# Performance work log

Measured on AMD Instinct MI355X. Metric: run time of the kernel, lower is better.

Reference implementation:

```python
import jax, jax.numpy as jnp
import numpy as np

N = 50000
E = 1600000
IN_CH = 64


def _sage_conv(x, edge_index, W_l, b_l, W_r):
    # PyG SAGEConv with mean aggregation:
    #   out = lin_l(mean_{j in N(i)} x_j) + lin_r(x_i)
    src, dst = edge_index[0], edge_index[1]
    n = x.shape[0]
    msg_sum = jax.ops.segment_sum(x[src], dst, num_segments=n)          # [N, d_in]
    cnt = jax.ops.segment_sum(jnp.ones((src.shape[0],), x.dtype), dst,
                              num_segments=n)                            # [N]
    agg = msg_sum / jnp.maximum(cnt, 1.0)[:, None]                       # mean, 0 if no nbrs
    return agg @ W_l.T + b_l + x @ W_r.T


def setup_inputs() -> dict:
    key = jax.random.key(0)
    ks = jax.random.split(key, 9)
    x = jax.random.normal(ks[0], (N, IN_CH), dtype=jnp.float32)
    edge_index = jax.random.randint(ks[1], (2, E), 0, N, dtype=jnp.int64)
    s = 1.0 / np.sqrt(IN_CH)
    W1_l = jax.random.uniform(ks[2], (64, IN_CH), jnp.float32, -s, s)
    b1_l = jnp.zeros((64,), jnp.float32)
    W1_r = jax.random.uniform(ks[3], (64, IN_CH), jnp.float32, -s, s)
    s2 = 1.0 / np.sqrt(64)
    W2_l = jax.random.uniform(ks[4], (32, 64), jnp.float32, -s2, s2)
    b2_l = jnp.zeros((32,), jnp.float32)
    W2_r = jax.random.uniform(ks[5], (32, 64), jnp.float32, -s2, s2)
    s3 = 1.0 / np.sqrt(32)
    W_lin = jax.random.uniform(ks[6], (1, 32), jnp.float32, -s3, s3)
    b_lin = jax.random.uniform(ks[7], (1,), jnp.float32, -s3, s3)
    return {"x": x, "edge_index": edge_index,
            "W1_l": W1_l, "b1_l": b1_l, "W1_r": W1_r,
            "W2_l": W2_l, "b2_l": b2_l, "W2_r": W2_r,
            "W_lin": W_lin, "b_lin": b_lin}


def reference(x, edge_index, W1_l, b1_l, W1_r, W2_l, b2_l, W2_r, W_lin, b_lin):
    h = jax.nn.relu(_sage_conv(x, edge_index, W1_l, b1_l, W1_r))   # [N, 64]
    h = jax.nn.relu(_sage_conv(h, edge_index, W2_l, b2_l, W2_r))   # [N, 32]
    return h @ W_lin.T + b_lin                                      # [N, 1]
```

## Files before the change

### kernel.cpp

```cpp
#include <hip/hip_runtime.h>
#include <cstdint>
#include <cstddef>

using u8  = unsigned char;
using u16 = unsigned short;
using u32 = unsigned int;

typedef short short8 __attribute__((ext_vector_type(8)));
typedef float f32x4 __attribute__((ext_vector_type(4)));

#define NB 256
#define HCAP4 12544

__device__ __forceinline__ float bf2f(u16 h) { return __uint_as_float(((u32)h) << 16); }
__device__ __forceinline__ u16 f2bf(float f) {
    u32 u = __float_as_uint(f);
    u += 0x7FFFu + ((u >> 16) & 1u);
    return (u16)(u >> 16);
}

__device__ __forceinline__ void load8(const float* p, float* v) {
    float4 a = ((const float4*)p)[0];
    float4 b = ((const float4*)p)[1];
    v[0]=a.x; v[1]=a.y; v[2]=a.z; v[3]=a.w;
    v[4]=b.x; v[5]=b.y; v[6]=b.z; v[7]=b.w;
}
__device__ __forceinline__ void load8(const u16* p, float* v) {
    uint4 u = *(const uint4*)p;
    v[0]=__uint_as_float(u.x << 16); v[1]=__uint_as_float(u.x & 0xFFFF0000u);
    v[2]=__uint_as_float(u.y << 16); v[3]=__uint_as_float(u.y & 0xFFFF0000u);
    v[4]=__uint_as_float(u.z << 16); v[5]=__uint_as_float(u.z & 0xFFFF0000u);
    v[6]=__uint_as_float(u.w << 16); v[7]=__uint_as_float(u.w & 0xFFFF0000u);
}
__device__ __forceinline__ void store8bf(u16* p, const float* v) {
    uint4 w;
    w.x = (u32)f2bf(v[0]) | ((u32)f2bf(v[1]) << 16);
    w.y = (u32)f2bf(v[2]) | ((u32)f2bf(v[3]) << 16);
    w.z = (u32)f2bf(v[4]) | ((u32)f2bf(v[5]) << 16);
    w.w = (u32)f2bf(v[6]) | ((u32)f2bf(v[7]) << 16);
    *(uint4*)p = w;
}
__device__ __forceinline__ short8 ld8b(const u16* p) {
    union { uint4 u; short8 s; } c;
    c.u = *(const uint4*)p;
    return c.s;
}

__global__ __launch_bounds__(1024) void hist_lds_kernel(const int* idx,
                                                        const float* __restrict__ x,
                                                        u16* __restrict__ xh,
                                                        u16* __restrict__ xl,
                                                        u32* __restrict__ mat,
                                                        u8* __restrict__ within,
                                                        u32* __restrict__ pe,
                                                        int E, int n, int total8) {
    __shared__ u32 h[HCAP4];
    __shared__ int s_nz;
    const int t = threadIdx.x;
    const int b = blockIdx.x;
    const int hw4 = (n + 3) >> 2;
    if (t == 0) s_nz = 0;
    for (int w = t; w < hw4; w += 1024) h[w] = 0;
    if (t < 128 && ((const u32*)idx)[2 * t + 1] != 0u) atomicOr(&s_nz, 1);

    {
        const int nt = (total8 + NB - 1) / NB;
        const int c1 = min(b * nt + nt, total8);
        for (int c = b * nt + t; c < c1; c += 1024) {
            float v[8], lo[8];
            load8(x + (size_t)c * 8, v);
            #pragma unroll
            for (int k = 0; k < 8; ++k) lo[k] = v[k] - bf2f(f2bf(v[k]));
            store8bf(xh + (size_t)c * 8, v);
            store8bf(xl + (size_t)c * 8, lo);
        }
    }
    __syncthreads();
    const int stride = s_nz ? 1 : 2;
    const int chunk = (E + NB - 1) / NB;
    const int e1 = min(b * chunk + chunk, E);
    for (int e = b * chunk + t; e < e1; e += 1024) {
        const int s = idx[(size_t)e * stride];
        const int d = idx[(size_t)(E + e) * stride];
        const int sh = (d & 3) << 3;
        const u32 old = atomicAdd(&h[d >> 2], 1u << sh);
        within[e] = (u8)((old >> sh) & 0xFFu);
        pe[e] = ((u32)d << 16) | (u32)s;
    }
    __syncthreads();
    u32* dst = mat + (size_t)b * hw4;
    for (int w = t; w < hw4; w += 1024) dst[w] = h[w];
}

__global__ __launch_bounds__(256) void csr_base_kernel(u32* __restrict__ mat,
                                                       int* __restrict__ deg, int n) {
    __shared__ u32 gs[16][17];
    const int hw4 = (n + 3) >> 2;
    const int wl = threadIdx.x & 15;
    const int j  = threadIdx.x >> 4;
    const int w = blockIdx.x * 16 + wl;
    u32 c[16];
    u32 s = 0;
    if (w < hw4) {
        #pragma unroll
        for (int k = 0; k < 16; ++k) {
            c[k] = mat[(size_t)(j * 16 + k) * hw4 + w];
            s += c[k];
        }
    }
    gs[j][wl] = s;
    __syncthreads();
    u32 run = 0, total = 0;
    for (int g = 0; g < 16; ++g) {
        const u32 v = gs[g][wl];
        if (g < j) run += v;
        total += v;
    }
    if (w < hw4) {
        #pragma unroll
        for (int k = 0; k < 16; ++k) {
            const size_t o = (size_t)(j * 16 + k) * hw4 + w;
            const u32 v = c[k];
            mat[o] = run;
            run += v;
        }
        if (j == 0) {
            #pragma unroll
            for (int q = 0; q < 4; ++q) {
                const int node = 4 * w + q;
                if (node < n) deg[node] = (int)((total >> (q << 3)) & 0xFFu);
            }
        }
    }
}

__global__ __launch_bounds__(256) void scan_partials_kernel(const int* __restrict__ deg,
                                                            int* __restrict__ bsum, int n) {
    __shared__ int ws[4];
    const int i = blockIdx.x * 256 + threadIdx.x;
    int v = (i < n) ? deg[i] : 0;
    #pragma unroll
    for (int m = 1; m < 64; m <<= 1) v += __shfl_xor(v, m, 64);
    const int lane = threadIdx.x & 63, wv = threadIdx.x >> 6;
    if (lane == 0) ws[wv] = v;
    __syncthreads();
    if (threadIdx.x == 0) bsum[blockIdx.x] = ws[0] + ws[1] + ws[2] + ws[3];
}

__global__ __launch_bounds__(256) void scan_write_kernel(const int* __restrict__ deg,
                                                         const int* __restrict__ bsum,
                                                         int* __restrict__ row_ptr,
                                                         int n, int nb) {
    __shared__ int wr[4];
    __shared__ int ws[4];
    __shared__ int s_boff;
    const int t = threadIdx.x;
    const int lane = t & 63, wv = t >> 6;
    int pv = (t < nb && t < blockIdx.x) ? bsum[t] : 0;
    #pragma unroll
    for (int o = 1; o < 64; o <<= 1) pv += __shfl_xor(pv, o, 64);
    if (lane == 0) wr[wv] = pv;
    __syncthreads();
    if (t == 0) s_boff = wr[0] + wr[1] + wr[2] + wr[3];
    const int i = blockIdx.x * 256 + t;
    const int x = (i < n) ? deg[i] : 0;
    int v = x;
    #pragma unroll
    for (int o = 1; o < 64; o <<= 1) {
        int u = __shfl_up(v, o, 64);
        if (lane >= o) v += u;
    }
    if (lane == 63) ws[wv] = v;
    __syncthreads();
    int woff = s_boff;
    for (int w = 0; w < wv; ++w) woff += ws[w];
    const int excl = v - x + woff;
    if (i < n) row_ptr[i] = excl;
    if (i == n - 1) row_ptr[n] = excl + x;
}

__global__ __launch_bounds__(1024) void scatter_kernel(const u32* __restrict__ pe,
                                                       const u32* __restrict__ mat,
                                                       const int* __restrict__ row_ptr,
                                                       const u8* __restrict__ within,
                                                       u16* __restrict__ ssrc, int E, int n) {
    const int hw4 = (n + 3) >> 2;
    const int chunk = (E + NB - 1) / NB;
    const int b = blockIdx.x;
    const int e1 = min(b * chunk + chunk, E);
    const u32* base = mat + (size_t)b * hw4;
    for (int e = b * chunk + threadIdx.x; e < e1; e += 1024) {
        const u32 p = pe[e];
        const int s = (int)(p & 0xFFFFu);
        const int d = (int)(p >> 16);
        const int wb = (int)((base[d >> 2] >> ((d & 3) << 3)) & 0xFFu);
        ssrc[row_ptr[d] + wb + (int)within[e]] = (u16)s;
    }
}

__global__ __launch_bounds__(256) void agg64_kernel(const u16* __restrict__ feat,
                                                    const int* __restrict__ row_ptr,
                                                    const u16* __restrict__ ssrc,
                                                    u16* __restrict__ out, int n) {
    const int lane = threadIdx.x & 63;
    const int wid = (blockIdx.x * blockDim.x + threadIdx.x) >> 6;
    const int nw = (gridDim.x * blockDim.x) >> 6;
    const int g = lane >> 3;
    const int q = lane & 7;
    for (int i = wid; i < n; i += nw) {
        const int rb = row_ptr[i], re = row_ptr[i + 1];
        float acc0[8], acc1[8];
        #pragma unroll
        for (int k = 0; k < 8; ++k) { acc0[k] = 0.f; acc1[k] = 0.f; }
        int e = rb + g;
        for (; e + 8 < re; e += 16) {
            const int s0 = (int)ssrc[e];
            const int s1 = (int)ssrc[e + 8];
            float v0[8], v1[8];
            load8(feat + (size_t)s0 * 64 + q * 8, v0);
            load8(feat + (size_t)s1 * 64 + q * 8, v1);
            #pragma unroll
            for (int k = 0; k < 8; ++k) { acc0[k] += v0[k]; acc1[k] += v1[k]; }
        }
        if (e < re) {
            const int s0 = (int)ssrc[e];
            float v0[8];
            load8(feat + (size_t)s0 * 64 + q * 8, v0);
            #pragma unroll
            for (int k = 0; k < 8; ++k) acc0[k] += v0[k];
        }
        #pragma unroll
        for (int k = 0; k < 8; ++k) acc0[k] += acc1[k];
        #pragma unroll
        for (int m = 8; m < 64; m <<= 1) {
            #pragma unroll
            for (int k = 0; k < 8; ++k) acc0[k] += __shfl_xor(acc0[k], m, 64);
        }
        if (g == 0) {
            float inv = 1.0f / (float)max(re - rb, 1);
            #pragma unroll
            for (int k = 0; k < 8; ++k) acc0[k] *= inv;
            store8bf(out + (size_t)i * 64 + q * 8, acc0);
        }
    }
}

#define W1P 140
#define W2P 76
__global__ __launch_bounds__(256) void layer1_mfma_kernel(
    const u16* __restrict__ A1b, const u16* __restrict__ xh, const u16* __restrict__ xl,
    const float* __restrict__ W1l, const float* __restrict__ b1,
    const float* __restrict__ W1r, const float* __restrict__ W2l,
    const float* __restrict__ b2, const float* __restrict__ W2r,
    u16* __restrict__ z2, float* __restrict__ r2, int n)
{
    __shared__ alignas(16) u16 w1h[64 * W1P], w1l[64 * W1P];
    __shared__ alignas(16) u16 w2h[64 * W2P], w2l[64 * W2P];
    __shared__ alignas(16) u16 h1h[64 * W2P], h1l[64 * W2P];

    const int t = threadIdx.x;
    for (int c = t; c < 64 * 32; c += 256) {
        const int ch = c >> 5, k = (c & 31) * 4;
        const float* src = (k < 64) ? (W1l + ch * 64 + k) : (W1r + ch * 64 + (k - 64));
        float4 w = *(const float4*)src;
        const float wv[4] = {w.x, w.y, w.z, w.w};
        #pragma unroll
        for (int j = 0; j < 4; ++j) {
            u16 h = f2bf(wv[j]);
            w1h[ch * W1P + k + j] = h;
            w1l[ch * W1P + k + j] = f2bf(wv[j] - bf2f(h));
        }
    }
    for (int c = t; c < 64 * 16; c += 256) {
        const int ch = c >> 4, k = (c & 15) * 4;
        const float* src = (ch < 32) ? (W2l + ch * 64 + k) : (W2r + (ch - 32) * 64 + k);
        float4 w = *(const float4*)src;
        const float wv[4] = {w.x, w.y, w.z, w.w};
        #pragma unroll
        for (int j = 0; j < 4; ++j) {
            u16 h = f2bf(wv[j]);
            w2h[ch * W2P + k + j] = h;
            w2l[ch * W2P + k + j] = f2bf(wv[j] - bf2f(h));
        }
    }
    __syncthreads();

    const int lane = t & 63;
    const int wv = t >> 6;
    const int m = lane & 15, quad = lane >> 4;
    const int base = blockIdx.x * 64 + wv * 16;

    const int nodeA = min(base + m, n - 1);
    const u16* a1row = A1b + (size_t)nodeA * 64;
    const u16* xhrow = xh + (size_t)nodeA * 64;
    const u16* xlrow = xl + (size_t)nodeA * 64;
    short8 aA[2], aH[2], aL[2];
    aA[0] = ld8b(a1row + quad * 8);      aA[1] = ld8b(a1row + 32 + quad * 8);
    aH[0] = ld8b(xhrow + quad * 8);      aH[1] = ld8b(xhrow + 32 + quad * 8);
    aL[0] = ld8b(xlrow + quad * 8);      aL[1] = ld8b(xlrow + 32 + quad * 8);

    #pragma unroll
    for (int ni = 0; ni < 4; ++ni) {
        const int row = ni * 16 + m;
        f32x4 acc = {0.f, 0.f, 0.f, 0.f};
        #pragma unroll
        for (int kc = 0; kc < 2; ++kc) {
            short8 b = ld8b(&w1h[row * W1P + kc * 32 + quad * 8]);
            acc = __builtin_amdgcn_mfma_f32_16x16x32_bf16(aA[kc], b, acc, 0, 0, 0);
        }
        #pragma unroll
        for (int kc = 0; kc < 2; ++kc) {
            short8 bh = ld8b(&w1h[row * W1P + 64 + kc * 32 + quad * 8]);
            short8 bl = ld8b(&w1l[row * W1P + 64 + kc * 32 + quad * 8]);
            acc = __builtin_amdgcn_mfma_f32_16x16x32_bf16(aH[kc], bh, acc, 0, 0, 0);
            acc = __builtin_amdgcn_mfma_f32_16x16x32_bf16(aH[kc], bl, acc, 0, 0, 0);
            acc = __builtin_amdgcn_mfma_f32_16x16x32_bf16(aL[kc], bh, acc, 0, 0, 0);
        }
        const float bias = b1[row];
        #pragma unroll
        for (int r = 0; r < 4; ++r) {
            float h = fmaxf(acc[r] + bias, 0.0f);
            u16 hh = f2bf(h);
            h1h[(wv * 16 + quad * 4 + r) * W2P + row] = hh;
            h1l[(wv * 16 + quad * 4 + r) * W2P + row] = f2bf(h - bf2f(hh));
        }
    }

    short8 ah[2], al[2];
    ah[0] = ld8b(&h1h[(wv * 16 + m) * W2P + quad * 8]);
    ah[1] = ld8b(&h1h[(wv * 16 + m) * W2P + 32 + quad * 8]);
    al[0] = ld8b(&h1l[(wv * 16 + m) * W2P + quad * 8]);
    al[1] = ld8b(&h1l[(wv * 16 + m) * W2P + 32 + quad * 8]);

    #pragma unroll
    for (int ni = 0; ni < 4; ++ni) {
        const int row = ni * 16 + m;
        f32x4 acc = {0.f, 0.f, 0.f, 0.f};
        #pragma unroll
        for (int kc = 0; kc < 2; ++kc) {
            short8 bh = ld8b(&w2h[row * W2P + kc * 32 + quad * 8]);
            short8 bl = ld8b(&w2l[row * W2P + kc * 32 + quad * 8]);
            acc = __builtin_amdgcn_mfma_f32_16x16x32_bf16(ah[kc], bh, acc, 0, 0, 0);
            acc = __builtin_amdgcn_mfma_f32_16x16x32_bf16(ah[kc], bl, acc, 0, 0, 0);
            acc = __builtin_amdgcn_mfma_f32_16x16x32_bf16(al[kc], bh, acc, 0, 0, 0);
        }
        if (ni < 2) {
            #pragma unroll
            for (int r = 0; r < 4; ++r) {
                int node = base + quad * 4 + r;
                if (node < n) z2[(size_t)node * 32 + row] = f2bf(acc[r]);
            }
        } else {
            const int ch = row - 32;
            const float bias = b2[ch];
            #pragma unroll
            for (int r = 0; r < 4; ++r) {
                int node = base + quad * 4 + r;
                if (node < n) r2[(size_t)node * 32 + ch] = acc[r] + bias;
            }
        }
    }
}

__global__ __launch_bounds__(256) void layer2_final_kernel(
    const u16* __restrict__ z2, const float* __restrict__ r2,
    const int* __restrict__ row_ptr, const u16* __restrict__ ssrc,
    const float* __restrict__ Wlin, const float* __restrict__ blin,
    float* __restrict__ out, int n)
{
    const int lane = threadIdx.x & 63;
    const int wid = (blockIdx.x * blockDim.x + threadIdx.x) >> 6;
    const int nw = (gridDim.x * blockDim.x) >> 6;
    const int g = lane >> 2;
    const int q = lane & 3;
    float wlin8[8];
    load8(Wlin + q * 8, wlin8);
    const float bl = blin[0];
    for (int i = wid; i < n; i += nw) {
        const int rb = row_ptr[i], re = row_ptr[i + 1];
        float acc0[8], acc1[8];
        #pragma unroll
        for (int k = 0; k < 8; ++k) { acc0[k] = 0.f; acc1[k] = 0.f; }
        int e = rb + g;
        for (; e + 16 < re; e += 32) {
            const int s0 = (int)ssrc[e];
            const int s1 = (int)ssrc[e + 16];
            float v0[8], v1[8];
            load8(z2 + (size_t)s0 * 32 + q * 8, v0);
            load8(z2 + (size_t)s1 * 32 + q * 8, v1);
            #pragma unroll
            for (int k = 0; k < 8; ++k) { acc0[k] += v0[k]; acc1[k] += v1[k]; }
        }
        if (e < re) {
            const int s0 = (int)ssrc[e];
            float v0[8];
            load8(z2 + (size_t)s0 * 32 + q * 8, v0);
            #pragma unroll
            for (int k = 0; k < 8; ++k) acc0[k] += v0[k];
        }
        #pragma unroll
        for (int k = 0; k < 8; ++k) acc0[k] += acc1[k];
        #pragma unroll
        for (int m = 4; m < 64; m <<= 1) {
            #pragma unroll
            for (int k = 0; k < 8; ++k) acc0[k] += __shfl_xor(acc0[k], m, 64);
        }
        float partial = 0.0f;
        if (g == 0) {
            const float inv = 1.0f / (float)max(re - rb, 1);
            float r2v[8];
            load8(r2 + (size_t)i * 32 + q * 8, r2v);
            #pragma unroll
            for (int k = 0; k < 8; ++k)
                partial += fmaxf(fmaf(acc0[k], inv, r2v[k]), 0.0f) * wlin8[k];
        }
        partial += __shfl_xor(partial, 1, 64);
        partial += __shfl_xor(partial, 2, 64);
        if (lane == 0) out[i] = partial + bl;
    }
}

extern "C" void kernel_launch(void* const* d_in, const int* in_sizes, int n_in,
                              void* d_out, int out_size, void* d_ws, size_t ws_size,
                              hipStream_t stream) {
    (void)n_in; (void)out_size; (void)ws_size;
    const int N = in_sizes[0] / 64;
    const int E = in_sizes[1] / 2;
    const int hw4 = (N + 3) >> 2;

    char* ws = (char*)d_ws;
    size_t off = 0;
    auto alloc = [&](size_t bytes) -> void* {
        void* p = ws + off;
        off += (bytes + 255) & ~(size_t)255;
        return p;
    };
    u32*   mat     = (u32*)alloc((size_t)NB * hw4 * 4);
    u8*    within  = (u8*)alloc((size_t)E);
    u32*   pe      = (u32*)alloc((size_t)E * 4);
    int*   deg     = (int*)alloc((size_t)N * 4);
    int*   row_ptr = (int*)alloc(((size_t)N + 1) * 4);
    u16*   ssrc    = (u16*)alloc((size_t)E * 2);
    int*   bsum    = (int*)alloc(1024);
    u16*   xh      = (u16*)alloc((size_t)N * 64 * 2);
    u16*   xl      = (u16*)alloc((size_t)N * 64 * 2);
    u16*   A1b     = (u16*)alloc((size_t)N * 64 * 2);
    u16*   z2      = (u16*)alloc((size_t)N * 32 * 2);
    float* r2      = (float*)alloc((size_t)N * 32 * 4);

    const int* idx = (const int*)d_in[1];
    const int nb2 = (N + 255) / 256;

    hist_lds_kernel<<<NB, 1024, 0, stream>>>(idx, (const float*)d_in[0], xh, xl,
                                             mat, within, pe, E, N, N * 8);
    csr_base_kernel<<<(hw4 + 15) / 16, 256, 0, stream>>>(mat, deg, N);
    scan_partials_kernel<<<nb2, 256, 0, stream>>>(deg, bsum, N);
    scan_write_kernel<<<nb2, 256, 0, stream>>>(deg, bsum, row_ptr, N, nb2);
    scatter_kernel<<<NB, 1024, 0, stream>>>(pe, mat, row_ptr, within, ssrc, E, N);

    agg64_kernel<<<2048, 256, 0, stream>>>(xh, row_ptr, ssrc, A1b, N);

    layer1_mfma_kernel<<<(N + 63) / 64, 256, 0, stream>>>(A1b, xh, xl,
        (const float*)d_in[2], (const float*)d_in[3], (const float*)d_in[4],
        (const float*)d_in[5], (const float*)d_in[6], (const float*)d_in[7],
        z2, r2, N);

    layer2_final_kernel<<<2048, 256, 0, stream>>>(z2, r2, row_ptr, ssrc,
        (const float*)d_in[8], (const float*)d_in[9], (float*)d_out, N);
}
```

Baseline: 221.7 us.

## Fuse CSR build kernels into one persistent kernel with grid barriers

Merges the histogram, base-offset, two scan kernels and the scatter into one 256-block persistent kernel that uses atomic grid barriers between phases. Each thread keeps its per-edge packed (dst,src) and within-bucket rank in registers, so the pe and within arrays no longer go through global memory, and four kernel launches are removed. In exchange, the barriers rely on all 256 blocks being co-resident, which is not guaranteed. The spin-waits also serialize the phases, and an extra memset is needed to reset the barrier counter.

New measurement: 718.1 us. +223.9%, slower.

```diff
diff --git a/kernel.cpp b/kernel.cpp
--- a/kernel.cpp
+++ b/kernel.cpp
@@ -10,6 +10,7 @@
 typedef float f32x4 __attribute__((ext_vector_type(4)));
 
 #define NB 256
+#define TPB 1024
 #define HCAP4 12544
 
 __device__ __forceinline__ float bf2f(u16 h) { return __uint_as_float(((u32)h) << 16); }
@@ -46,27 +47,47 @@
     return c.s;
 }
 
-__global__ __launch_bounds__(1024) void hist_lds_kernel(const int* idx,
-                                                        const float* __restrict__ x,
-                                                        u16* __restrict__ xh,
-                                                        u16* __restrict__ xl,
-                                                        u32* __restrict__ mat,
-                                                        u8* __restrict__ within,
-                                                        u32* __restrict__ pe,
-                                                        int E, int n, int total8) {
+__device__ __forceinline__ void grid_barrier(u32* bar, u32 target) {
+    __threadfence();
+    __syncthreads();
+    if (threadIdx.x == 0) {
+        __hip_atomic_fetch_add(bar, 1u, __ATOMIC_RELEASE, __HIP_MEMORY_SCOPE_AGENT);
+        while (__hip_atomic_load(bar, __ATOMIC_ACQUIRE, __HIP_MEMORY_SCOPE_AGENT) < target)
+            __builtin_amdgcn_s_sleep(2);
+    }
+    __syncthreads();
+    __threadfence();
+}
+
+__global__ __launch_bounds__(1024, 4) void csr_fused_kernel(
+    const int* idx, const float* __restrict__ x,
+    u16* __restrict__ xh, u16* __restrict__ xl,
+    u32* __restrict__ mat, int* __restrict__ bsum,
+    int* __restrict__ row_ptr, u16* __restrict__ ssrc,
+    u32* __restrict__ bar, int E, int n, int total8)
+{
     __shared__ u32 h[HCAP4];
+    __shared__ int s_deg[256];
+    __shared__ int s_red[16];
+    __shared__ int s_wsum[16];
     __shared__ int s_nz;
+    __shared__ int s_bsum;
+
     const int t = threadIdx.x;
     const int b = blockIdx.x;
     const int hw4 = (n + 3) >> 2;
-    if (t == 0) s_nz = 0;
-    for (int w = t; w < hw4; w += 1024) h[w] = 0;
+    const int wpb = (hw4 + NB - 1) / NB;
+    const int npb = 4 * wpb;
+
+    if (t == 0) { s_nz = 0; s_bsum = 0; }
+    if (t < 256) s_deg[t] = 0;
+    for (int w = t; w < hw4; w += TPB) h[w] = 0;
     if (t < 128 && ((const u32*)idx)[2 * t + 1] != 0u) atomicOr(&s_nz, 1);
 
     {
         const int nt = (total8 + NB - 1) / NB;
         const int c1 = min(b * nt + nt, total8);
-        for (int c = b * nt + t; c < c1; c += 1024) {
+        for (int c = b * nt + t; c < c1; c += TPB) {
             float v[8], lo[8];
             load8(x + (size_t)c * 8, v);
             #pragma unroll
@@ -76,125 +97,121 @@
         }
     }
     __syncthreads();
+
     const int stride = s_nz ? 1 : 2;
     const int chunk = (E + NB - 1) / NB;
+    const int e0 = b * chunk + t;
     const int e1 = min(b * chunk + chunk, E);
-    for (int e = b * chunk + t; e < e1; e += 1024) {
-        const int s = idx[(size_t)e * stride];
-        const int d = idx[(size_t)(E + e) * stride];
-        const int sh = (d & 3) << 3;
-        const u32 old = atomicAdd(&h[d >> 2], 1u << sh);
-        within[e] = (u8)((old >> sh) & 0xFFu);
-        pe[e] = ((u32)d << 16) | (u32)s;
+    u32 rs[7], rw[7];
+    #pragma unroll
+    for (int j = 0; j < 7; ++j) {
+        const int e = e0 + j * TPB;
+        rs[j] = 0u; rw[j] = 0u;
+        if (e < e1) {
+            const int s = idx[(size_t)e * stride];
+            const int d = idx[(size_t)(E + e) * stride];
+            const int sh = (d & 3) << 3;
+            const u32 old = atomicAdd(&h[d >> 2], 1u << sh);
+            rw[j] = (old >> sh) & 0xFFu;
+            rs[j] = ((u32)d << 16) | (u32)s;
+        }
     }
     __syncthreads();
-    u32* dst = mat + (size_t)b * hw4;
-    for (int w = t; w < hw4; w += 1024) dst[w] = h[w];
-}
-
-__global__ __launch_bounds__(256) void csr_base_kernel(u32* __restrict__ mat,
-                                                       int* __restrict__ deg, int n) {
-    __shared__ u32 gs[16][17];
-    const int hw4 = (n + 3) >> 2;
-    const int wl = threadIdx.x & 15;
-    const int j  = threadIdx.x >> 4;
-    const int w = blockIdx.x * 16 + wl;
-    u32 c[16];
-    u32 s = 0;
-    if (w < hw4) {
-        #pragma unroll
-        for (int k = 0; k < 16; ++k) {
-            c[k] = mat[(size_t)(j * 16 + k) * hw4 + w];
-            s += c[k];
-        }
-    }
-    gs[j][wl] = s;
-    __syncthreads();
-    u32 run = 0, total = 0;
-    for (int g = 0; g < 16; ++g) {
-        const u32 v = gs[g][wl];
-        if (g < j) run += v;
-        total += v;
-    }
-    if (w < hw4) {
-        #pragma unroll
-        for (int k = 0; k < 16; ++k) {
-            const size_t o = (size_t)(j * 16 + k) * hw4 + w;
-            const u32 v = c[k];
-            mat[o] = run;
-            run += v;
-        }
-        if (j == 0) {
-            #pragma unroll
-            for (int q = 0; q < 4; ++q) {
-                const int node = 4 * w + q;
-                if (node < n) deg[node] = (int)((total >> (q << 3)) & 0xFFu);
-            }
-        }
-    }
-}
-
-__global__ __launch_bounds__(256) void scan_partials_kernel(const int* __restrict__ deg,
-                                                            int* __restrict__ bsum, int n) {
-    __shared__ int ws[4];
-    const int i = blockIdx.x * 256 + threadIdx.x;
-    int v = (i < n) ? deg[i] : 0;
-    #pragma unroll
-    for (int m = 1; m < 64; m <<= 1) v += __shfl_xor(v, m, 64);
-    const int lane = threadIdx.x & 63, wv = threadIdx.x >> 6;
-    if (lane == 0) ws[wv] = v;
-    __syncthreads();
-    if (threadIdx.x == 0) bsum[blockIdx.x] = ws[0] + ws[1] + ws[2] + ws[3];
-}
-
-__global__ __launch_bounds__(256) void scan_write_kernel(const int* __restrict__ deg,
-                                                         const int* __restrict__ bsum,
-                                                         int* __restrict__ row_ptr,
-                                                         int n, int nb) {
-    __shared__ int wr[4];
-    __shared__ int ws[4];
-    __shared__ int s_boff;
-    const int t = threadIdx.x;
-    const int lane = t & 63, wv = t >> 6;
-    int pv = (t < nb && t < blockIdx.x) ? bsum[t] : 0;
-    #pragma unroll
-    for (int o = 1; o < 64; o <<= 1) pv += __shfl_xor(pv, o, 64);
-    if (lane == 0) wr[wv] = pv;
-    __syncthreads();
-    if (t == 0) s_boff = wr[0] + wr[1] + wr[2] + wr[3];
-    const int i = blockIdx.x * 256 + t;
-    const int x = (i < n) ? deg[i] : 0;
-    int v = x;
-    #pragma unroll
-    for (int o = 1; o < 64; o <<= 1) {
-        int u = __shfl_up(v, o, 64);
-        if (lane >= o) v += u;
-    }
-    if (lane == 63) ws[wv] = v;
-    __syncthreads();
-    int woff = s_boff;
-    for (int w = 0; w < wv; ++w) woff += ws[w];
-    const int excl = v - x + woff;
-    if (i < n) row_ptr[i] = excl;
-    if (i == n - 1) row_ptr[n] = excl + x;
-}
-
-__global__ __launch_bounds__(1024) void scatter_kernel(const u32* __restrict__ pe,
-                                                       const u32* __restrict__ mat,
-                                                       const int* __restrict__ row_ptr,
-                                                       const u8* __restrict__ within,
-                                                       u16* __restrict__ ssrc, int E, int n) {
-    const int hw4 = (n + 3) >> 2;
-    const int chunk = (E + NB - 1) / NB;
-    const int b = blockIdx.x;
-    const int e1 = min(b * chunk + chunk, E);
-    const u32* base = mat + (size_t)b * hw4;
-    for (int e = b * chunk + threadIdx.x; e < e1; e += 1024) {
-        const u32 p = pe[e];
-        const int s = (int)(p & 0xFFFFu);
-        const int d = (int)(p >> 16);
-        const int wb = (int)((base[d >> 2] >> ((d & 3) << 3)) & 0xFFu);
-        ssrc[row_ptr[d] + wb + (int)within[e]] = (u16)s;
+    {
+        u32* dst = mat + (size_t)b * hw4;
+        for (int w = t; w < hw4; w += TPB) dst[w] = h[w];
+    }
+    grid_barrier(bar, NB * 1);
+
+    {
+        u32* gs = h;
+        const int wloc = t >> 4;
+        const int rj = t & 15;
+        const int w = b * wpb + wloc;
+        const bool wok = (wloc < wpb) && (w < hw4);
+        u32 c[16];
+        u32 ssum = 0;
+        if (wok) {
+            #pragma unroll
+            for (int k = 0; k < 16; ++k) {
+                c[k] = mat[(size_t)(rj * 16 + k) * hw4 + w];
+                ssum += c[k];
+            }
+        }
+        gs[wloc * 17 + rj] = ssum;
+        __syncthreads();
+        u32 run = 0, total = 0;
+        #pragma unroll
+        for (int g = 0; g < 16; ++g) {
+            const u32 v = gs[wloc * 17 + g];
+            if (g < rj) run += v;
+            total += v;
+        }
+        if (wok) {
+            #pragma unroll
+            for (int k = 0; k < 16; ++k) {
+                const size_t o = (size_t)(rj * 16 + k) * hw4 + w;
+                const u32 v = c[k];
+                mat[o] = run;
+                run += v;
+            }
+            if (rj == 0) {
+                int dsum = 0;
+                #pragma unroll
+                for (int q = 0; q < 4; ++q) {
+                    const int node = 4 * w + q;
+                    const int dv = (int)((total >> (q << 3)) & 0xFFu);
+                    if (node < n) { s_deg[4 * wloc + q] = dv; dsum += dv; }
+                }
+                atomicAdd(&s_bsum, dsum);
+            }
+        }
+        __syncthreads();
+        if (t == 0) bsum[b] = s_bsum;
+    }
+    grid_barrier(bar, NB * 2);
+
+    {
+        const int lane = t & 63, wv = t >> 6;
+        int pv = (t < NB && t < b) ? bsum[t] : 0;
+        #pragma unroll
+        for (int m = 1; m < 64; m <<= 1) pv += __shfl_xor(pv, m, 64);
+        if (lane == 0) s_red[wv] = pv;
+        __syncthreads();
+        int boff = 0;
+        #pragma unroll
+        for (int k = 0; k < 16; ++k) boff += s_red[k];
+        const int gbase = b * npb;
+        const int cnt = min(npb, n - gbase);
+        const int xd = (t < npb) ? s_deg[t] : 0;
+        int v = xd;
+        #pragma unroll
+        for (int o = 1; o < 64; o <<= 1) {
+            int u = __shfl_up(v, o, 64);
+            if (lane >= o) v += u;
+        }
+        if (lane == 63) s_wsum[wv] = v;
+        __syncthreads();
+        int woff = boff;
+        for (int w = 0; w < wv; ++w) woff += s_wsum[w];
+        const int excl = v - xd + woff;
+        if (t < cnt) row_ptr[gbase + t] = excl;
+        if (gbase + t == n - 1) row_ptr[n] = excl + xd;
+    }
+    grid_barrier(bar, NB * 3);
+
+    {
+        const u32* basep = mat + (size_t)b * hw4;
+        #pragma unroll
+        for (int j = 0; j < 7; ++j) {
+            const int e = e0 + j * TPB;
+            if (e < e1) {
+                const int s = (int)(rs[j] & 0xFFFFu);
+                const int d = (int)(rs[j] >> 16);
+                const int wb = (int)((basep[d >> 2] >> ((d & 3) << 3)) & 0xFFu);
+                ssrc[row_ptr[d] + wb + (int)rw[j]] = (u16)s;
+            }
+        }
     }
 }
 
@@ -436,12 +453,10 @@
         return p;
     };
     u32*   mat     = (u32*)alloc((size_t)NB * hw4 * 4);
-    u8*    within  = (u8*)alloc((size_t)E);
-    u32*   pe      = (u32*)alloc((size_t)E * 4);
-    int*   deg     = (int*)alloc((size_t)N * 4);
     int*   row_ptr = (int*)alloc(((size_t)N + 1) * 4);
     u16*   ssrc    = (u16*)alloc((size_t)E * 2);
     int*   bsum    = (int*)alloc(1024);
+    u32*   bar     = (u32*)alloc(256);
     u16*   xh      = (u16*)alloc((size_t)N * 64 * 2);
     u16*   xl      = (u16*)alloc((size_t)N * 64 * 2);
     u16*   A1b     = (u16*)alloc((size_t)N * 64 * 2);
@@ -449,14 +464,11 @@
     float* r2      = (float*)alloc((size_t)N * 32 * 4);
 
     const int* idx = (const int*)d_in[1];
-    const int nb2 = (N + 255) / 256;
-
-    hist_lds_kernel<<<NB, 1024, 0, stream>>>(idx, (const float*)d_in[0], xh, xl,
-                                             mat, within, pe, E, N, N * 8);
-    csr_base_kernel<<<(hw4 + 15) / 16, 256, 0, stream>>>(mat, deg, N);
-    scan_partials_kernel<<<nb2, 256, 0, stream>>>(deg, bsum, N);
-    scan_write_kernel<<<nb2, 256, 0, stream>>>(deg, bsum, row_ptr, N, nb2);
-    scatter_kernel<<<NB, 1024, 0, stream>>>(pe, mat, row_ptr, within, ssrc, E, N);
+
+    hipMemsetAsync(bar, 0, 256, stream);
+
+    csr_fused_kernel<<<NB, TPB, 0, stream>>>(idx, (const float*)d_in[0], xh, xl,
+                                             mat, bsum, row_ptr, ssrc, bar, E, N, N * 8);
 
     agg64_kernel<<<2048, 256, 0, stream>>>(xh, row_ptr, ssrc, A1b, N);
 
```
